# Kernel tuning notes

Measured on AMD Instinct MI355X. Metric: run time of the kernel, lower is better.

Reference implementation:

```python
import jax, jax.numpy as jnp
import numpy as np

N_FEATURES = 1024
N_HEADS = 16
D_ATTN = 64


def setup_inputs() -> dict:
    key = jax.random.key(0)
    k_x, k_qkv, k_pw, k_pb = jax.random.split(key, 4)
    B, S = 2, 2048
    x = jax.random.normal(k_x, (B, S, N_FEATURES), dtype=jnp.float32)
    # torch nn.Linear weights are [out, in]; init scale ~ 1/sqrt(in)
    w_qkv = jax.random.normal(k_qkv, (3 * N_HEADS * D_ATTN, N_FEATURES), dtype=jnp.float32) / np.sqrt(N_FEATURES)
    w_proj = jax.random.normal(k_pw, (N_FEATURES, N_HEADS * D_ATTN), dtype=jnp.float32) / np.sqrt(N_HEADS * D_ATTN)
    b_proj = jax.random.normal(k_pb, (N_FEATURES,), dtype=jnp.float32) / np.sqrt(N_HEADS * D_ATTN)
    return {"x": x, "w_qkv": w_qkv, "w_proj": w_proj, "b_proj": b_proj}


def reference(x, w_qkv, w_proj, b_proj):
    B, S, F = x.shape
    H, D = N_HEADS, D_ATTN
    # fused QKV projection (bias=False): [B,S,3*H*D]
    qkv = jnp.einsum('bsf,of->bso', x, w_qkv)
    qkv = qkv.reshape(B, S, 3, H, D)
    q = jnp.transpose(qkv[:, :, 0], (0, 2, 1, 3))  # [B,H,S,D]
    k = jnp.transpose(qkv[:, :, 1], (0, 2, 1, 3))
    v = jnp.transpose(qkv[:, :, 2], (0, 2, 1, 3))
    scale = 1.0 / jnp.sqrt(jnp.asarray(D, dtype=x.dtype))
    scores = jnp.einsum('bhqd,bhkd->bhqk', q, k) * scale  # [B,H,S,S]
    attn = jax.nn.softmax(scores, axis=-1)
    out = jnp.einsum('bhqk,bhkd->bhqd', attn, v)  # [B,H,S,D]
    out = jnp.transpose(out, (0, 2, 1, 3)).reshape(B, S, H * D)
    # output projection (dropout is identity in eval mode)
    return jnp.einsum('bsm,fm->bsf', out, w_proj) + b_proj
```

## Files before the change

kernel.cpp:

```cpp
#include <hip/hip_runtime.h>
#include <hip/hip_bf16.h>
#include <math.h>

#define BATCH 2
#define SEQ 2048
#define NFEAT 1024
#define NHEAD 16
#define DHEAD 64
#define MROWS (BATCH * SEQ)
#define NQKV (3 * NHEAD * DHEAD)

typedef __attribute__((ext_vector_type(8))) short short8;
typedef __attribute__((ext_vector_type(4))) float floatx4;
typedef __attribute__((ext_vector_type(16))) float floatx16;
typedef __attribute__((ext_vector_type(4))) unsigned int uintx4;

#define CEXP 0.18033688f

__device__ __forceinline__ unsigned short f2bf(float f) {
    unsigned int u = __float_as_uint(f);
    u += 0x7fff + ((u >> 16) & 1);
    return (unsigned short)(u >> 16);
}

__device__ __forceinline__ float fast_exp2(float x) {
    return __builtin_amdgcn_exp2f(x);
}

__device__ __forceinline__ uint pack_bf16x2(float lo, float hi) {
    float2 t; t.x = lo; t.y = hi;
    __hip_bfloat162 h = __float22bfloat162_rn(t);
    union { __hip_bfloat162 h; uint u; } c; c.h = h;
    return c.u;
}

__device__ __forceinline__ void async16(const void* g, void* l) {
    __builtin_amdgcn_global_load_lds(
        (const __attribute__((address_space(1))) void*)g,
        (__attribute__((address_space(3))) void*)l, 16, 0, 0);
}

__global__ void cvt_swz(const float* __restrict__ x, const float* __restrict__ wq,
                        const float* __restrict__ wp,
                        ushort* __restrict__ xb, ushort* __restrict__ wqb,
                        ushort* __restrict__ wpb) {
    const int NX = MROWS * NFEAT / 4, NWQ = NQKV * NFEAT / 4, NWP = NFEAT * NFEAT / 4;
    int i = blockIdx.x * blockDim.x + threadIdx.x;
    if (i >= NX + NWQ + NWP) return;
    const float* src; ushort* dst; int idx4;
    if (i < NX)            { src = x;  dst = xb;  idx4 = i; }
    else if (i < NX + NWQ) { src = wq; dst = wqb; idx4 = i - NX; }
    else                   { src = wp; dst = wpb; idx4 = i - NX - NWQ; }
    float4 v = ((const float4*)src)[idx4];
    ushort4 o;
    o.x = f2bf(v.x); o.y = f2bf(v.y); o.z = f2bf(v.z); o.w = f2bf(v.w);
    const int e = idx4 * 4;
    const int k = e & (NFEAT - 1);
    const int row = e >> 10;
    const int kp = (k & ~31) | (((((k >> 3) & 3) ^ ((row >> 1) & 3))) << 3) | (k & 7);
    *(ushort4*)(dst + (size_t)row * NFEAT + kp) = o;
}

__global__ __launch_bounds__(256, 3)
void gemm_qkv(const ushort* __restrict__ A, const ushort* __restrict__ W,
              ushort* __restrict__ qb, ushort* __restrict__ kb, ushort* __restrict__ vtb) {
    __shared__ ushort smem[16384];
    ushort* As = smem;
    ushort* Bs = smem + 8192;
    const int tid = threadIdx.x;
    const int wave = tid >> 6, lane = tid & 63;
    const int id = blockIdx.x;
    const int xcd = id & 7, slot = id >> 3;
    const int by = (xcd >> 1) * 8 + slot / 12;
    const int bx = (xcd & 1) * 12 + slot % 12;
    const int m0 = by * 128, n0 = bx * 128;
    const int wm = (wave >> 1) * 64, wn = (wave & 1) * 64;
    const int lr = lane & 15, lg = lane >> 4;
    const int kswz = (lg ^ ((lr >> 1) & 3)) * 8;

    floatx4 acc[4][4] = {};

    for (int k0 = 0; k0 < NFEAT; k0 += 64) {
#pragma unroll
        for (int q = 0; q < 4; ++q) {
            const int s = q * 256 + tid;
            const int row = s >> 3, kc = (s & 7) * 8;
            async16(A + (size_t)(m0 + row) * NFEAT + k0 + kc, (void*)(As + s * 8));
            async16(W + (size_t)(n0 + row) * NFEAT + k0 + kc, (void*)(Bs + s * 8));
        }
        __syncthreads();
#pragma unroll
        for (int kk = 0; kk < 2; ++kk) {
            short8 a[4], b[4];
#pragma unroll
            for (int i = 0; i < 4; ++i)
                a[i] = *(const short8*)(As + (wm + i * 16 + lr) * 64 + kk * 32 + kswz);
#pragma unroll
            for (int j = 0; j < 4; ++j)
                b[j] = *(const short8*)(Bs + (wn + j * 16 + lr) * 64 + kk * 32 + kswz);
#pragma unroll
            for (int i = 0; i < 4; ++i)
#pragma unroll
                for (int j = 0; j < 4; ++j)
                    acc[i][j] = __builtin_amdgcn_mfma_f32_16x16x32_bf16(a[i], b[j], acc[i][j], 0, 0, 0);
        }
        __syncthreads();
    }

    const int t = n0 >> 10;
    const int bidx = m0 >> 11;
    if (t < 2) {
#pragma unroll
        for (int i = 0; i < 4; ++i)
#pragma unroll
            for (int j = 0; j < 4; ++j)
#pragma unroll
                for (int r = 0; r < 4; ++r) {
                    const int m = m0 + wm + i * 16 + lg * 4 + r;
                    const int n = n0 + wn + j * 16 + lr;
                    const int s = m & (SEQ - 1);
                    const int rem = n & 1023, h = rem >> 6, d = rem & 63;
                    if (t == 0) {
                        qb[((size_t)(bidx * NHEAD + h) * SEQ + s) * DHEAD + d] =
                            f2bf(acc[i][j][r] * CEXP);
                    } else {
                        const int dcol = ((((d >> 3) ^ (s & 7)) << 3)) | (d & 7);
                        kb[((size_t)(bidx * NHEAD + h) * SEQ + s) * DHEAD + dcol] =
                            f2bf(acc[i][j][r]);
                    }
                }
    } else {
#pragma unroll
        for (int hhalf = 0; hhalf < 2; ++hhalf) {
            if ((wm >> 6) == hhalf) {
#pragma unroll
                for (int i = 0; i < 4; ++i) {
                    const int chunk = i * 2 + (lg >> 1);
#pragma unroll
                    for (int j = 0; j < 4; ++j) {
                        const int n = wn + j * 16 + lr;
                        uint2 pk;
                        pk.x = pack_bf16x2(acc[i][j][0], acc[i][j][1]);
                        pk.y = pack_bf16x2(acc[i][j][2], acc[i][j][3]);
                        *(uint2*)(smem + n * 64 + ((chunk ^ (n & 7)) * 8) + (lg & 1) * 4) = pk;
                    }
                }
            }
            __syncthreads();
            const int s_base = (m0 & (SEQ - 1)) + hhalf * 64;
#pragma unroll
            for (int it = 0; it < 4; ++it) {
                const int n_r = (tid >> 3) + it * 32;
                const int p = tid & 7;
                short8 rowv = *(const short8*)(smem + n_r * 64 + p * 8);
                const int nglob = n0 + n_r;
                const int d = nglob & 63, hh = (nglob & 1023) >> 6;
                *(short8*)(vtb + ((size_t)(bidx * NHEAD + hh) * DHEAD + d) * SEQ + s_base + p * 8) = rowv;
            }
            __syncthreads();
        }
    }
}

__global__ __launch_bounds__(256, 2)
void gemm_proj(const ushort* __restrict__ A, const ushort* __restrict__ W,
               const float* __restrict__ bias, float* __restrict__ Cout) {
    __shared__ ushort As[128 * 64];
    __shared__ ushort Bs[64 * 64];
    const int tid = threadIdx.x;
    const int wave = tid >> 6, lane = tid & 63;
    const int id = blockIdx.x;
    const int xcd = id & 7, slot = id >> 3;
    const int by = (xcd >> 1) * 8 + (slot >> 3);
    const int bx = (xcd & 1) * 8 + (slot & 7);
    const int m0 = by * 128, n0 = bx * 64;
    const int wm = (wave >> 1) * 64, wn = (wave & 1) * 32;
    const int lr = lane & 15, lg = lane >> 4;
    const int kswz = (lg ^ ((lr >> 1) & 3)) * 8;

    floatx4 acc[4][2] = {};

    for (int k0 = 0; k0 < NFEAT; k0 += 64) {
#pragma unroll
        for (int q = 0; q < 4; ++q) {
            const int s = q * 256 + tid;
            const int row = s >> 3, kc = (s & 7) * 8;
            async16(A + (size_t)(m0 + row) * NFEAT + k0 + kc, (void*)(As + s * 8));
        }
#pragma unroll
        for (int q = 0; q < 2; ++q) {
            const int s = q * 256 + tid;
            const int row = s >> 3, kc = (s & 7) * 8;
            async16(W + (size_t)(n0 + row) * NFEAT + k0 + kc, (void*)(Bs + s * 8));
        }
        __syncthreads();
#pragma unroll
        for (int kk = 0; kk < 2; ++kk) {
            short8 a[4], b[2];
#pragma unroll
            for (int i = 0; i < 4; ++i)
                a[i] = *(const short8*)(As + (wm + i * 16 + lr) * 64 + kk * 32 + kswz);
#pragma unroll
            for (int j = 0; j < 2; ++j)
                b[j] = *(const short8*)(Bs + (wn + j * 16 + lr) * 64 + kk * 32 + kswz);
#pragma unroll
            for (int i = 0; i < 4; ++i)
#pragma unroll
                for (int j = 0; j < 2; ++j)
                    acc[i][j] = __builtin_amdgcn_mfma_f32_16x16x32_bf16(a[i], b[j], acc[i][j], 0, 0, 0);
        }
        __syncthreads();
    }

#pragma unroll
    for (int i = 0; i < 4; ++i)
#pragma unroll
        for (int j = 0; j < 2; ++j)
#pragma unroll
            for (int r = 0; r < 4; ++r) {
                const int m = m0 + wm + i * 16 + lg * 4 + r;
                const int n = n0 + wn + j * 16 + lr;
                Cout[(size_t)m * NFEAT + n] = acc[i][j][r] + bias[n];
            }
}

__global__ __launch_bounds__(512, 4)
void flash_attn(const ushort* __restrict__ qb, const ushort* __restrict__ kb,
                const ushort* __restrict__ vtb, ushort* __restrict__ aob) {
    const int id = blockIdx.x;
    const int xcd = id & 7, slot = id >> 3;
    const int bh = xcd + 8 * (slot >> 4);
    const int qt = slot & 15;
    const int tid = threadIdx.x, wave = tid >> 6, lane = tid & 63;
    const int l31 = lane & 31, l5 = lane >> 5;
    const int swz = lane & 7;
    const int kvh = wave >> 2;
    const int qw = wave & 3;

    __shared__ ushort Ks[2][2][64 * 64];
    __shared__ ushort Vs[2][2][64 * 64];

    const ushort* Qb = qb + (size_t)bh * SEQ * DHEAD;
    const ushort* Kb = kb + (size_t)bh * SEQ * DHEAD;
    const ushort* Vt = vtb + (size_t)bh * DHEAD * SEQ;

    const int q0 = qt * 128 + qw * 32;

    short8 qf[4];
#pragma unroll
    for (int kw = 0; kw < 4; ++kw)
        qf[kw] = *(const short8*)(Qb + (size_t)(q0 + l31) * DHEAD + kw * 16 + l5 * 8);

    const int kofs = tid * 8;
    const size_t vrow = (size_t)(tid >> 3) * SEQ;
    const int vcol = (tid & 7) * 8;

    const ushort* KsW = &Ks[kvh][0][0];
    const ushort* VsW = &Vs[kvh][0][0];

    floatx16 acc_o[2] = {};
    float l_lane = 0.0f;

#define FLASH_PREFETCH(BUF, KV)                                                     \
    {                                                                               \
        const int kv_ = (KV);                                                       \
        async16(Kb + (size_t)kv_ * DHEAD + kofs,            (void*)(Ks[0][BUF] + kofs)); \
        async16(Kb + (size_t)(1024 + kv_) * DHEAD + kofs,   (void*)(Ks[1][BUF] + kofs)); \
        async16(Vt + vrow + kv_ + vcol,                     (void*)(Vs[0][BUF] + kofs)); \
        async16(Vt + vrow + 1024 + kv_ + vcol,              (void*)(Vs[1][BUF] + kofs)); \
    }

#define FLASH_COMPUTE(BUF)                                                          \
    {                                                                               \
        floatx16 st[2] = {};                                                        \
        __builtin_amdgcn_s_setprio(1);                                              \
        _Pragma("unroll")                                                           \
        for (int kw = 0; kw < 4; ++kw) {                                            \
            _Pragma("unroll")                                                       \
            for (int i = 0; i < 2; ++i) {                                           \
                short8 kf = *(const short8*)(KsW + (BUF) * 4096 + (i * 32 + l31) * 64 + \
                                             (((kw * 2 + l5) ^ swz) * 8));          \
                st[i] = __builtin_amdgcn_mfma_f32_32x32x16_bf16(kf, qf[kw], st[i], 0, 0, 0); \
            }                                                                       \
        }                                                                           \
        __builtin_amdgcn_s_setprio(0);                                              \
        uintx4 pa[4];                                                               \
        _Pragma("unroll")                                                           \
        for (int i = 0; i < 2; ++i) {                                               \
            uint P2[8];                                                             \
            _Pragma("unroll")                                                       \
            for (int rr = 0; rr < 8; ++rr) {                                        \
                const float p0 = fast_exp2(st[i][rr * 2]);                          \
                const float p1 = fast_exp2(st[i][rr * 2 + 1]);                      \
                l_lane += p0 + p1;                                                  \
                P2[rr] = pack_bf16x2(p0, p1);                                       \
            }                                                                       \
            _Pragma("unroll")                                                       \
            for (int r3 = 0; r3 < 2; ++r3) {                                        \
                _Pragma("unroll")                                                   \
                for (int r1 = 0; r1 < 2; ++r1) {                                    \
                    uint a = P2[r3 * 4 + r1];                            \
                    uint b = P2[r3 * 4 + 2 + r1];                        \
                    asm volatile("v_permlane32_swap_b32 %0, %1" : "+v"(a), "+v"(b)); \
                    pa[i * 2 + r3][r1] = a;               \
                    pa[i * 2 + r3][2 + r1] = b;           \
                }                                                                   \
            }                                                                       \
        }                                                                           \
        __builtin_amdgcn_s_setprio(1);                                              \
        _Pragma("unroll")                                                           \
        for (int kk = 0; kk < 4; ++kk) {                                            \
            const short8 paf = *(const short8*)&pa[kk];                             \
            _Pragma("unroll")                                                       \
            for (int j2 = 0; j2 < 2; ++j2) {                                        \
                short8 vf = *(const short8*)(VsW + (BUF) * 4096 + (j2 * 32 + l31) * 64 + \
                                             (((kk * 2 + l5) ^ swz) * 8));          \
                acc_o[j2] = __builtin_amdgcn_mfma_f32_32x32x16_bf16(paf, vf, acc_o[j2], 0, 0, 0); \
            }                                                                       \
        }                                                                           \
        __builtin_amdgcn_s_setprio(0);                                              \
    }

    FLASH_PREFETCH(0, 0)

    for (int kt = 0; kt < 1024; kt += 128) {
        __syncthreads();
        FLASH_PREFETCH(1, kt + 64)
        FLASH_COMPUTE(0)
        __syncthreads();
        if (kt + 128 < 1024)
            FLASH_PREFETCH(0, kt + 128)
        FLASH_COMPUTE(1)
    }
#undef FLASH_PREFETCH
#undef FLASH_COMPUTE

    __syncthreads();
    float* mrg = (float*)&Ks[0][0][0];
    if (wave >= 4) {
        float* p = mrg + (size_t)(wave - 4) * 2304 + lane * 36;
#pragma unroll
        for (int j2 = 0; j2 < 2; ++j2)
#pragma unroll
            for (int r4 = 0; r4 < 4; ++r4) {
                floatx4 v;
                v[0] = acc_o[j2][r4 * 4 + 0];
                v[1] = acc_o[j2][r4 * 4 + 1];
                v[2] = acc_o[j2][r4 * 4 + 2];
                v[3] = acc_o[j2][r4 * 4 + 3];
                *(floatx4*)(p + j2 * 16 + r4 * 4) = v;
            }
        p[32] = l_lane;
    }
    __syncthreads();
    if (wave < 4) {
        const float* p = mrg + (size_t)wave * 2304 + lane * 36;
#pragma unroll
        for (int j2 = 0; j2 < 2; ++j2)
#pragma unroll
            for (int r4 = 0; r4 < 4; ++r4) {
                floatx4 v = *(const floatx4*)(p + j2 * 16 + r4 * 4);
#pragma unroll
                for (int e = 0; e < 4; ++e)
                    acc_o[j2][r4 * 4 + e] += v[e];
            }
        l_lane += p[32];

        l_lane += __shfl_xor(l_lane, 32);
        const float invl = 1.0f / l_lane;

        const int b = bh >> 4, h = bh & 15;
#pragma unroll
        for (int r = 0; r < 16; ++r) {
            const int qrow = (r & 3) + 4 * l5 + 8 * (r >> 2);
            const float il = __shfl(invl, qrow);
            const int srow = b * SEQ + q0 + qrow;
            const int key = (srow >> 1) & 3;
#pragma unroll
            for (int j2 = 0; j2 < 2; ++j2) {
                const int d = j2 * 32 + l31;
                const int dsw = (d & ~31) | ((((d >> 3) & 3) ^ key) << 3) | (d & 7);
                aob[(size_t)srow * (NHEAD * DHEAD) + h * DHEAD + dsw] = f2bf(acc_o[j2][r] * il);
            }
        }
    }
}

extern "C" void kernel_launch(void* const* d_in, const int* in_sizes, int n_in,
                              void* d_out, int out_size, void* d_ws, size_t ws_size,
                              hipStream_t stream) {
    const float* x      = (const float*)d_in[0];
    const float* w_qkv  = (const float*)d_in[1];
    const float* w_proj = (const float*)d_in[2];
    const float* b_proj = (const float*)d_in[3];
    float* out = (float*)d_out;

    ushort* ws = (ushort*)d_ws;
    ushort* xb     = ws;
    ushort* wqkvb  = xb + (size_t)MROWS * NFEAT;
    ushort* wprojb = wqkvb + (size_t)NQKV * NFEAT;
    ushort* qb     = wprojb + (size_t)NFEAT * NFEAT;
    ushort* kb     = qb + (size_t)MROWS * NFEAT;
    ushort* vtb    = kb + (size_t)MROWS * NFEAT;
    ushort* aob    = vtb + (size_t)MROWS * NFEAT;

    {
        const int total = (MROWS * NFEAT + NQKV * NFEAT + NFEAT * NFEAT) / 4;
        cvt_swz<<<(total + 255) / 256, 256, 0, stream>>>(x, w_qkv, w_proj, xb, wqkvb, wprojb);
    }

    {
        gemm_qkv<<<768, 256, 0, stream>>>(xb, wqkvb, qb, kb, vtb);
    }

    {
        flash_attn<<<512, 512, 0, stream>>>(qb, kb, vtb, aob);
    }

    {
        gemm_proj<<<512, 256, 0, stream>>>(aob, wprojb, b_proj, out);
    }
}
```

Before: 176.2 us.

## Halve flash-attention waves, each wave handles 64 query rows sharing K/V fragments

The attention block drops from 8 to 4 waves. Each wave now processes two 32-row query sub-tiles, so every K and V fragment read from LDS feeds two MFMAs instead of one. This halves LDS read traffic per unit of compute and doubles register use per wave for accumulators and Q fragments. Each thread now issues twice as many async prefetch loads, and the merge step is reworked for the new wave layout. The risk is lower occupancy and less latency hiding with fewer waves per block.

```diff
diff --git a/kernel.cpp b/kernel.cpp
--- a/kernel.cpp
+++ b/kernel.cpp
@@ -224,7 +224,7 @@
             }
 }
 
-__global__ __launch_bounds__(512, 4)
+__global__ __launch_bounds__(256, 2)
 void flash_attn(const ushort* __restrict__ qb, const ushort* __restrict__ kb,
                 const ushort* __restrict__ vtb, ushort* __restrict__ aob) {
     const int id = blockIdx.x;
@@ -234,45 +234,52 @@
     const int tid = threadIdx.x, wave = tid >> 6, lane = tid & 63;
     const int l31 = lane & 31, l5 = lane >> 5;
     const int swz = lane & 7;
-    const int kvh = wave >> 2;
-    const int qw = wave & 3;
-
-    __shared__ ushort Ks[2][2][64 * 64];
-    __shared__ ushort Vs[2][2][64 * 64];
+    const int kvh = wave >> 1;
+    const int qw = wave & 1;
+
+    __shared__ __align__(16) ushort sm[32768];
+    ushort* Ksp = sm;
+    ushort* Vsp = sm + 16384;
 
     const ushort* Qb = qb + (size_t)bh * SEQ * DHEAD;
     const ushort* Kb = kb + (size_t)bh * SEQ * DHEAD;
     const ushort* Vt = vtb + (size_t)bh * DHEAD * SEQ;
 
-    const int q0 = qt * 128 + qw * 32;
-
-    short8 qf[4];
-#pragma unroll
-    for (int kw = 0; kw < 4; ++kw)
-        qf[kw] = *(const short8*)(Qb + (size_t)(q0 + l31) * DHEAD + kw * 16 + l5 * 8);
+    const int q0 = qt * 128 + qw * 64;
+
+    short8 qf[2][4];
+#pragma unroll
+    for (int qh = 0; qh < 2; ++qh)
+#pragma unroll
+        for (int kw = 0; kw < 4; ++kw)
+            qf[qh][kw] = *(const short8*)(Qb + (size_t)(q0 + qh * 32 + l31) * DHEAD + kw * 16 + l5 * 8);
 
     const int kofs = tid * 8;
     const size_t vrow = (size_t)(tid >> 3) * SEQ;
     const int vcol = (tid & 7) * 8;
 
-    const ushort* KsW = &Ks[kvh][0][0];
-    const ushort* VsW = &Vs[kvh][0][0];
-
-    floatx16 acc_o[2] = {};
-    float l_lane = 0.0f;
+    const ushort* KsW = Ksp + kvh * 8192;
+    const ushort* VsW = Vsp + kvh * 8192;
+
+    floatx16 acc_o[2][2] = {};
+    float l_lane[2] = {0.0f, 0.0f};
 
 #define FLASH_PREFETCH(BUF, KV)                                                     \
     {                                                                               \
         const int kv_ = (KV);                                                       \
-        async16(Kb + (size_t)kv_ * DHEAD + kofs,            (void*)(Ks[0][BUF] + kofs)); \
-        async16(Kb + (size_t)(1024 + kv_) * DHEAD + kofs,   (void*)(Ks[1][BUF] + kofs)); \
-        async16(Vt + vrow + kv_ + vcol,                     (void*)(Vs[0][BUF] + kofs)); \
-        async16(Vt + vrow + 1024 + kv_ + vcol,              (void*)(Vs[1][BUF] + kofs)); \
+        async16(Kb + (size_t)kv_ * DHEAD + kofs,                 (void*)(Ksp + (BUF) * 4096 + kofs)); \
+        async16(Kb + (size_t)kv_ * DHEAD + 2048 + kofs,          (void*)(Ksp + (BUF) * 4096 + 2048 + kofs)); \
+        async16(Kb + (size_t)(1024 + kv_) * DHEAD + kofs,        (void*)(Ksp + 8192 + (BUF) * 4096 + kofs)); \
+        async16(Kb + (size_t)(1024 + kv_) * DHEAD + 2048 + kofs, (void*)(Ksp + 8192 + (BUF) * 4096 + 2048 + kofs)); \
+        async16(Vt + vrow + kv_ + vcol,                          (void*)(Vsp + (BUF) * 4096 + kofs)); \
+        async16(Vt + 32 * SEQ + vrow + kv_ + vcol,               (void*)(Vsp + (BUF) * 4096 + 2048 + kofs)); \
+        async16(Vt + vrow + 1024 + kv_ + vcol,                   (void*)(Vsp + 8192 + (BUF) * 4096 + kofs)); \
+        async16(Vt + 32 * SEQ + vrow + 1024 + kv_ + vcol,        (void*)(Vsp + 8192 + (BUF) * 4096 + 2048 + kofs)); \
     }
 
 #define FLASH_COMPUTE(BUF)                                                          \
     {                                                                               \
-        floatx16 st[2] = {};                                                        \
+        floatx16 st[2][2] = {};                                                     \
         __builtin_amdgcn_s_setprio(1);                                              \
         _Pragma("unroll")                                                           \
         for (int kw = 0; kw < 4; ++kw) {                                            \
@@ -280,42 +287,48 @@
             for (int i = 0; i < 2; ++i) {                                           \
                 short8 kf = *(const short8*)(KsW + (BUF) * 4096 + (i * 32 + l31) * 64 + \
                                              (((kw * 2 + l5) ^ swz) * 8));          \
-                st[i] = __builtin_amdgcn_mfma_f32_32x32x16_bf16(kf, qf[kw], st[i], 0, 0, 0); \
+                st[0][i] = __builtin_amdgcn_mfma_f32_32x32x16_bf16(kf, qf[0][kw], st[0][i], 0, 0, 0); \
+                st[1][i] = __builtin_amdgcn_mfma_f32_32x32x16_bf16(kf, qf[1][kw], st[1][i], 0, 0, 0); \
             }                                                                       \
         }                                                                           \
         __builtin_amdgcn_s_setprio(0);                                              \
-        uintx4 pa[4];                                                               \
+        uintx4 pa[2][4];                                                            \
         _Pragma("unroll")                                                           \
-        for (int i = 0; i < 2; ++i) {                                               \
-            uint P2[8];                                                             \
+        for (int qh = 0; qh < 2; ++qh) {                                            \
             _Pragma("unroll")                                                       \
-            for (int rr = 0; rr < 8; ++rr) {                                        \
-                const float p0 = fast_exp2(st[i][rr * 2]);                          \
-                const float p1 = fast_exp2(st[i][rr * 2 + 1]);                      \
-                l_lane += p0 + p1;                                                  \
-                P2[rr] = pack_bf16x2(p0, p1);                                       \
-            }                                                                       \
-            _Pragma("unroll")                                                       \
-            for (int r3 = 0; r3 < 2; ++r3) {                                        \
+            for (int i = 0; i < 2; ++i) {                                           \
+                uint P2[8];                                                         \
                 _Pragma("unroll")                                                   \
-                for (int r1 = 0; r1 < 2; ++r1) {                                    \
-                    uint a = P2[r3 * 4 + r1];                            \
-                    uint b = P2[r3 * 4 + 2 + r1];                        \
-                    asm volatile("v_permlane32_swap_b32 %0, %1" : "+v"(a), "+v"(b)); \
-                    pa[i * 2 + r3][r1] = a;               \
-                    pa[i * 2 + r3][2 + r1] = b;           \
+                for (int rr = 0; rr < 8; ++rr) {                                    \
+                    const float p0 = fast_exp2(st[qh][i][rr * 2]);                  \
+                    const float p1 = fast_exp2(st[qh][i][rr * 2 + 1]);              \
+                    l_lane[qh] += p0 + p1;                                          \
+                    P2[rr] = pack_bf16x2(p0, p1);                                   \
+                }                                                                   \
+                _Pragma("unroll")                                                   \
+                for (int r3 = 0; r3 < 2; ++r3) {                                    \
+                    _Pragma("unroll")                                               \
+                    for (int r1 = 0; r1 < 2; ++r1) {                                \
+                        uint a = P2[r3 * 4 + r1];                        \
+                        uint b = P2[r3 * 4 + 2 + r1];                    \
+                        asm volatile("v_permlane32_swap_b32 %0, %1" : "+v"(a), "+v"(b)); \
+                        pa[qh][i * 2 + r3][r1] = a;       \
+                        pa[qh][i * 2 + r3][2 + r1] = b;   \
+                    }                                                               \
                 }                                                                   \
             }                                                                       \
         }                                                                           \
         __builtin_amdgcn_s_setprio(1);                                              \
         _Pragma("unroll")                                                           \
         for (int kk = 0; kk < 4; ++kk) {                                            \
-            const short8 paf = *(const short8*)&pa[kk];                             \
+            const short8 paf0 = *(const short8*)&pa[0][kk];                         \
+            const short8 paf1 = *(const short8*)&pa[1][kk];                         \
             _Pragma("unroll")                                                       \
             for (int j2 = 0; j2 < 2; ++j2) {                                        \
                 short8 vf = *(const short8*)(VsW + (BUF) * 4096 + (j2 * 32 + l31) * 64 + \
                                              (((kk * 2 + l5) ^ swz) * 8));          \
-                acc_o[j2] = __builtin_amdgcn_mfma_f32_32x32x16_bf16(paf, vf, acc_o[j2], 0, 0, 0); \
+                acc_o[0][j2] = __builtin_amdgcn_mfma_f32_32x32x16_bf16(paf0, vf, acc_o[0][j2], 0, 0, 0); \
+                acc_o[1][j2] = __builtin_amdgcn_mfma_f32_32x32x16_bf16(paf1, vf, acc_o[1][j2], 0, 0, 0); \
             }                                                                       \
         }                                                                           \
         __builtin_amdgcn_s_setprio(0);                                              \
@@ -336,51 +349,59 @@
 #undef FLASH_COMPUTE
 
     __syncthreads();
-    float* mrg = (float*)&Ks[0][0][0];
-    if (wave >= 4) {
-        float* p = mrg + (size_t)(wave - 4) * 2304 + lane * 36;
-#pragma unroll
-        for (int j2 = 0; j2 < 2; ++j2)
-#pragma unroll
-            for (int r4 = 0; r4 < 4; ++r4) {
-                floatx4 v;
-                v[0] = acc_o[j2][r4 * 4 + 0];
-                v[1] = acc_o[j2][r4 * 4 + 1];
-                v[2] = acc_o[j2][r4 * 4 + 2];
-                v[3] = acc_o[j2][r4 * 4 + 3];
-                *(floatx4*)(p + j2 * 16 + r4 * 4) = v;
-            }
-        p[32] = l_lane;
+    float* Mrg = (float*)sm;
+    if (kvh == 1) {
+        float* p = Mrg + (size_t)(qw * 64 + lane) * 68;
+#pragma unroll
+        for (int qh = 0; qh < 2; ++qh)
+#pragma unroll
+            for (int j2 = 0; j2 < 2; ++j2)
+#pragma unroll
+                for (int r4 = 0; r4 < 4; ++r4) {
+                    floatx4 v;
+                    v[0] = acc_o[qh][j2][r4 * 4 + 0];
+                    v[1] = acc_o[qh][j2][r4 * 4 + 1];
+                    v[2] = acc_o[qh][j2][r4 * 4 + 2];
+                    v[3] = acc_o[qh][j2][r4 * 4 + 3];
+                    *(floatx4*)(p + qh * 32 + j2 * 16 + r4 * 4) = v;
+                }
+        p[64] = l_lane[0];
+        p[65] = l_lane[1];
     }
     __syncthreads();
-    if (wave < 4) {
-        const float* p = mrg + (size_t)wave * 2304 + lane * 36;
-#pragma unroll
-        for (int j2 = 0; j2 < 2; ++j2)
-#pragma unroll
-            for (int r4 = 0; r4 < 4; ++r4) {
-                floatx4 v = *(const floatx4*)(p + j2 * 16 + r4 * 4);
-#pragma unroll
-                for (int e = 0; e < 4; ++e)
-                    acc_o[j2][r4 * 4 + e] += v[e];
-            }
-        l_lane += p[32];
-
-        l_lane += __shfl_xor(l_lane, 32);
-        const float invl = 1.0f / l_lane;
+    if (kvh == 0) {
+        const float* p = Mrg + (size_t)(qw * 64 + lane) * 68;
+#pragma unroll
+        for (int qh = 0; qh < 2; ++qh)
+#pragma unroll
+            for (int j2 = 0; j2 < 2; ++j2)
+#pragma unroll
+                for (int r4 = 0; r4 < 4; ++r4) {
+                    floatx4 v = *(const floatx4*)(p + qh * 32 + j2 * 16 + r4 * 4);
+#pragma unroll
+                    for (int e = 0; e < 4; ++e)
+                        acc_o[qh][j2][r4 * 4 + e] += v[e];
+                }
+        l_lane[0] += p[64];
+        l_lane[1] += p[65];
 
         const int b = bh >> 4, h = bh & 15;
 #pragma unroll
-        for (int r = 0; r < 16; ++r) {
-            const int qrow = (r & 3) + 4 * l5 + 8 * (r >> 2);
-            const float il = __shfl(invl, qrow);
-            const int srow = b * SEQ + q0 + qrow;
-            const int key = (srow >> 1) & 3;
-#pragma unroll
-            for (int j2 = 0; j2 < 2; ++j2) {
-                const int d = j2 * 32 + l31;
-                const int dsw = (d & ~31) | ((((d >> 3) & 3) ^ key) << 3) | (d & 7);
-                aob[(size_t)srow * (NHEAD * DHEAD) + h * DHEAD + dsw] = f2bf(acc_o[j2][r] * il);
+        for (int qh = 0; qh < 2; ++qh) {
+            l_lane[qh] += __shfl_xor(l_lane[qh], 32);
+            const float invl = 1.0f / l_lane[qh];
+#pragma unroll
+            for (int r = 0; r < 16; ++r) {
+                const int qrow = (r & 3) + 4 * l5 + 8 * (r >> 2);
+                const float il = __shfl(invl, qrow);
+                const int srow = b * SEQ + q0 + qh * 32 + qrow;
+                const int key = (srow >> 1) & 3;
+#pragma unroll
+                for (int j2 = 0; j2 < 2; ++j2) {
+                    const int d = j2 * 32 + l31;
+                    const int dsw = (d & ~31) | ((((d >> 3) & 3) ^ key) << 3) | (d & 7);
+                    aob[(size_t)srow * (NHEAD * DHEAD) + h * DHEAD + dsw] = f2bf(acc_o[qh][j2][r] * il);
+                }
             }
         }
     }
@@ -414,7 +435,7 @@
     }
 
     {
-        flash_attn<<<512, 512, 0, stream>>>(qb, kb, vtb, aob);
+        flash_attn<<<512, 256, 0, stream>>>(qb, kb, vtb, aob);
     }
 
     {
```

Measured after the change: 180.6 us. +2.5%, slower.

## Drop LDS staging in flash attention and read K/V directly from global

Applied to the files above, without the earlier changes.

The attention kernel no longer stages K and V tiles in shared memory through double-buffered async copies. Each wave now loads its K and V MFMA fragments straight from global memory, relying on the existing swizzled layout and on L2/cache hits. Blocks shrink to four waves covering 64 queries, with twice as many blocks launched, and shared memory is kept only for the final merge of the two KV halves. This cuts LDS use and the copy pipeline, which allows more resident blocks. The cost is exposed global-load latency, no reuse of K/V tiles across waves in a block, and a barrier left inside the loop.

```diff
diff --git a/kernel.cpp b/kernel.cpp
--- a/kernel.cpp
+++ b/kernel.cpp
@@ -224,121 +224,88 @@
             }
 }
 
-__global__ __launch_bounds__(512, 4)
+__global__ __launch_bounds__(256, 4)
 void flash_attn(const ushort* __restrict__ qb, const ushort* __restrict__ kb,
                 const ushort* __restrict__ vtb, ushort* __restrict__ aob) {
     const int id = blockIdx.x;
     const int xcd = id & 7, slot = id >> 3;
-    const int bh = xcd + 8 * (slot >> 4);
-    const int qt = slot & 15;
+    const int bh = xcd + 8 * (slot >> 5);
+    const int qt2 = slot & 31;
     const int tid = threadIdx.x, wave = tid >> 6, lane = tid & 63;
     const int l31 = lane & 31, l5 = lane >> 5;
-    const int swz = lane & 7;
-    const int kvh = wave >> 2;
-    const int qw = wave & 3;
-
-    __shared__ ushort Ks[2][2][64 * 64];
-    __shared__ ushort Vs[2][2][64 * 64];
+    const int swz = l31 & 7;
+    const int kvh = wave >> 1;
+    const int qw = wave & 1;
+
+    __shared__ float mrg[2 * 64 * 36];
 
     const ushort* Qb = qb + (size_t)bh * SEQ * DHEAD;
-    const ushort* Kb = kb + (size_t)bh * SEQ * DHEAD;
-    const ushort* Vt = vtb + (size_t)bh * DHEAD * SEQ;
-
-    const int q0 = qt * 128 + qw * 32;
+    const ushort* Kb = kb + (size_t)bh * SEQ * DHEAD + (size_t)kvh * 1024 * DHEAD;
+    const ushort* Vt = vtb + (size_t)bh * DHEAD * SEQ + (size_t)kvh * 1024;
+
+    const int q0 = qt2 * 64 + qw * 32;
 
     short8 qf[4];
 #pragma unroll
     for (int kw = 0; kw < 4; ++kw)
         qf[kw] = *(const short8*)(Qb + (size_t)(q0 + l31) * DHEAD + kw * 16 + l5 * 8);
 
-    const int kofs = tid * 8;
-    const size_t vrow = (size_t)(tid >> 3) * SEQ;
-    const int vcol = (tid & 7) * 8;
-
-    const ushort* KsW = &Ks[kvh][0][0];
-    const ushort* VsW = &Vs[kvh][0][0];
-
     floatx16 acc_o[2] = {};
     float l_lane = 0.0f;
 
-#define FLASH_PREFETCH(BUF, KV)                                                     \
-    {                                                                               \
-        const int kv_ = (KV);                                                       \
-        async16(Kb + (size_t)kv_ * DHEAD + kofs,            (void*)(Ks[0][BUF] + kofs)); \
-        async16(Kb + (size_t)(1024 + kv_) * DHEAD + kofs,   (void*)(Ks[1][BUF] + kofs)); \
-        async16(Vt + vrow + kv_ + vcol,                     (void*)(Vs[0][BUF] + kofs)); \
-        async16(Vt + vrow + 1024 + kv_ + vcol,              (void*)(Vs[1][BUF] + kofs)); \
-    }
-
-#define FLASH_COMPUTE(BUF)                                                          \
-    {                                                                               \
-        floatx16 st[2] = {};                                                        \
-        __builtin_amdgcn_s_setprio(1);                                              \
-        _Pragma("unroll")                                                           \
-        for (int kw = 0; kw < 4; ++kw) {                                            \
-            _Pragma("unroll")                                                       \
-            for (int i = 0; i < 2; ++i) {                                           \
-                short8 kf = *(const short8*)(KsW + (BUF) * 4096 + (i * 32 + l31) * 64 + \
-                                             (((kw * 2 + l5) ^ swz) * 8));          \
-                st[i] = __builtin_amdgcn_mfma_f32_32x32x16_bf16(kf, qf[kw], st[i], 0, 0, 0); \
-            }                                                                       \
-        }                                                                           \
-        __builtin_amdgcn_s_setprio(0);                                              \
-        uintx4 pa[4];                                                               \
-        _Pragma("unroll")                                                           \
-        for (int i = 0; i < 2; ++i) {                                               \
-            uint P2[8];                                                             \
-            _Pragma("unroll")                                                       \
-            for (int rr = 0; rr < 8; ++rr) {                                        \
-                const float p0 = fast_exp2(st[i][rr * 2]);                          \
-                const float p1 = fast_exp2(st[i][rr * 2 + 1]);                      \
-                l_lane += p0 + p1;                                                  \
-                P2[rr] = pack_bf16x2(p0, p1);                                       \
-            }                                                                       \
-            _Pragma("unroll")                                                       \
-            for (int r3 = 0; r3 < 2; ++r3) {                                        \
-                _Pragma("unroll")                                                   \
-                for (int r1 = 0; r1 < 2; ++r1) {                                    \
-                    uint a = P2[r3 * 4 + r1];                            \
-                    uint b = P2[r3 * 4 + 2 + r1];                        \
-                    asm volatile("v_permlane32_swap_b32 %0, %1" : "+v"(a), "+v"(b)); \
-                    pa[i * 2 + r3][r1] = a;               \
-                    pa[i * 2 + r3][2 + r1] = b;           \
-                }                                                                   \
-            }                                                                       \
-        }                                                                           \
-        __builtin_amdgcn_s_setprio(1);                                              \
-        _Pragma("unroll")                                                           \
-        for (int kk = 0; kk < 4; ++kk) {                                            \
-            const short8 paf = *(const short8*)&pa[kk];                             \
-            _Pragma("unroll")                                                       \
-            for (int j2 = 0; j2 < 2; ++j2) {                                        \
-                short8 vf = *(const short8*)(VsW + (BUF) * 4096 + (j2 * 32 + l31) * 64 + \
-                                             (((kk * 2 + l5) ^ swz) * 8));          \
-                acc_o[j2] = __builtin_amdgcn_mfma_f32_32x32x16_bf16(paf, vf, acc_o[j2], 0, 0, 0); \
-            }                                                                       \
-        }                                                                           \
-        __builtin_amdgcn_s_setprio(0);                                              \
-    }
-
-    FLASH_PREFETCH(0, 0)
-
-    for (int kt = 0; kt < 1024; kt += 128) {
-        __syncthreads();
-        FLASH_PREFETCH(1, kt + 64)
-        FLASH_COMPUTE(0)
-        __syncthreads();
-        if (kt + 128 < 1024)
-            FLASH_PREFETCH(0, kt + 128)
-        FLASH_COMPUTE(1)
-    }
-#undef FLASH_PREFETCH
-#undef FLASH_COMPUTE
-
-    __syncthreads();
-    float* mrg = (float*)&Ks[0][0][0];
-    if (wave >= 4) {
-        float* p = mrg + (size_t)(wave - 4) * 2304 + lane * 36;
+    for (int kt = 0; kt < 1024; kt += 64) {
+        floatx16 st[2] = {};
+        __builtin_amdgcn_s_setprio(1);
+#pragma unroll
+        for (int kw = 0; kw < 4; ++kw) {
+#pragma unroll
+            for (int i = 0; i < 2; ++i) {
+                short8 kf = *(const short8*)(Kb + (size_t)(kt + i * 32 + l31) * DHEAD +
+                                             (((kw * 2 + l5) ^ swz) * 8));
+                st[i] = __builtin_amdgcn_mfma_f32_32x32x16_bf16(kf, qf[kw], st[i], 0, 0, 0);
+            }
+        }
+        __builtin_amdgcn_s_setprio(0);
+        uintx4 pa[4];
+#pragma unroll
+        for (int i = 0; i < 2; ++i) {
+            uint P2[8];
+#pragma unroll
+            for (int rr = 0; rr < 8; ++rr) {
+                const float p0 = fast_exp2(st[i][rr * 2]);
+                const float p1 = fast_exp2(st[i][rr * 2 + 1]);
+                l_lane += p0 + p1;
+                P2[rr] = pack_bf16x2(p0, p1);
+            }
+#pragma unroll
+            for (int r3 = 0; r3 < 2; ++r3) {
+#pragma unroll
+                for (int r1 = 0; r1 < 2; ++r1) {
+                    uint a = P2[r3 * 4 + r1];
+                    uint b = P2[r3 * 4 + 2 + r1];
+                    asm volatile("v_permlane32_swap_b32 %0, %1" : "+v"(a), "+v"(b));
+                    pa[i * 2 + r3][r1] = a;
+                    pa[i * 2 + r3][2 + r1] = b;
+                }
+            }
+        }
+        __builtin_amdgcn_s_setprio(1);
+#pragma unroll
+        for (int kk = 0; kk < 4; ++kk) {
+            const short8 paf = *(const short8*)&pa[kk];
+#pragma unroll
+            for (int j2 = 0; j2 < 2; ++j2) {
+                short8 vf = *(const short8*)(Vt + (size_t)(j2 * 32 + l31) * SEQ + kt +
+                                             (((kk * 2 + l5) ^ swz) * 8));
+                acc_o[j2] = __builtin_amdgcn_mfma_f32_32x32x16_bf16(paf, vf, acc_o[j2], 0, 0, 0);
+            }
+        }
+        __builtin_amdgcn_s_setprio(0);
+        __syncthreads();
+    }
+
+    float* p = mrg + (size_t)(qw * 64 + lane) * 36;
+    if (kvh == 1) {
 #pragma unroll
         for (int j2 = 0; j2 < 2; ++j2)
 #pragma unroll
@@ -353,8 +320,7 @@
         p[32] = l_lane;
     }
     __syncthreads();
-    if (wave < 4) {
-        const float* p = mrg + (size_t)wave * 2304 + lane * 36;
+    if (kvh == 0) {
 #pragma unroll
         for (int j2 = 0; j2 < 2; ++j2)
 #pragma unroll
@@ -414,7 +380,7 @@
     }
 
     {
-        flash_attn<<<512, 512, 0, stream>>>(qb, kb, vtb, aob);
+        flash_attn<<<1024, 256, 0, stream>>>(qb, kb, vtb, aob);
     }
 
     {
```

New measurement: 199.8 us. +13.4%, slower.

## Load V fragments directly from global memory instead of staging through LDS

Applied to the files above, without the earlier changes.

The flash-attention kernel stops copying V tiles into shared memory. Each wave now reads its V MFMA operands straight from global (transposed V) memory, with half of them issued early in the compute step to hide latency. Shared memory shrinks to the K buffers plus the merge scratch, which may allow more resident blocks. In exchange there is more global/L2 traffic, because each of the four q-waves reloads the same V data, and the loads sit on the critical path before the PV MFMAs.

```diff
diff --git a/kernel.cpp b/kernel.cpp
--- a/kernel.cpp
+++ b/kernel.cpp
@@ -233,16 +233,16 @@
     const int qt = slot & 15;
     const int tid = threadIdx.x, wave = tid >> 6, lane = tid & 63;
     const int l31 = lane & 31, l5 = lane >> 5;
-    const int swz = lane & 7;
+    const int swz = l31 & 7;
     const int kvh = wave >> 2;
     const int qw = wave & 3;
 
-    __shared__ ushort Ks[2][2][64 * 64];
-    __shared__ ushort Vs[2][2][64 * 64];
+    __shared__ __align__(16) char smraw[36864];
+    ushort* Ksp = (ushort*)smraw;
 
     const ushort* Qb = qb + (size_t)bh * SEQ * DHEAD;
     const ushort* Kb = kb + (size_t)bh * SEQ * DHEAD;
-    const ushort* Vt = vtb + (size_t)bh * DHEAD * SEQ;
+    const ushort* Vt = vtb + (size_t)bh * DHEAD * SEQ + (size_t)kvh * 1024;
 
     const int q0 = qt * 128 + qw * 32;
 
@@ -252,11 +252,7 @@
         qf[kw] = *(const short8*)(Qb + (size_t)(q0 + l31) * DHEAD + kw * 16 + l5 * 8);
 
     const int kofs = tid * 8;
-    const size_t vrow = (size_t)(tid >> 3) * SEQ;
-    const int vcol = (tid & 7) * 8;
-
-    const ushort* KsW = &Ks[kvh][0][0];
-    const ushort* VsW = &Vs[kvh][0][0];
+    const ushort* KsW = Ksp + kvh * 8192;
 
     floatx16 acc_o[2] = {};
     float l_lane = 0.0f;
@@ -264,14 +260,20 @@
 #define FLASH_PREFETCH(BUF, KV)                                                     \
     {                                                                               \
         const int kv_ = (KV);                                                       \
-        async16(Kb + (size_t)kv_ * DHEAD + kofs,            (void*)(Ks[0][BUF] + kofs)); \
-        async16(Kb + (size_t)(1024 + kv_) * DHEAD + kofs,   (void*)(Ks[1][BUF] + kofs)); \
-        async16(Vt + vrow + kv_ + vcol,                     (void*)(Vs[0][BUF] + kofs)); \
-        async16(Vt + vrow + 1024 + kv_ + vcol,              (void*)(Vs[1][BUF] + kofs)); \
-    }
-
-#define FLASH_COMPUTE(BUF)                                                          \
+        async16(Kb + (size_t)kv_ * DHEAD + kofs,          (void*)(Ksp + (BUF) * 4096 + kofs));        \
+        async16(Kb + (size_t)(1024 + kv_) * DHEAD + kofs, (void*)(Ksp + 8192 + (BUF) * 4096 + kofs)); \
+    }
+
+#define FLASH_COMPUTE(BUF, KV)                                                      \
     {                                                                               \
+                    \
+        short8 vgA[2][2];                                                           \
+        _Pragma("unroll")                                                           \
+        for (int kk = 0; kk < 2; ++kk)                                              \
+            _Pragma("unroll")                                                       \
+            for (int j2 = 0; j2 < 2; ++j2)                                          \
+                vgA[kk][j2] = *(const short8*)(Vt + (size_t)(j2 * 32 + l31) * SEQ + \
+                                               (KV) + (((kk * 2 + l5) ^ swz) * 8)); \
         floatx16 st[2] = {};                                                        \
         __builtin_amdgcn_s_setprio(1);                                              \
         _Pragma("unroll")                                                           \
@@ -313,8 +315,9 @@
             const short8 paf = *(const short8*)&pa[kk];                             \
             _Pragma("unroll")                                                       \
             for (int j2 = 0; j2 < 2; ++j2) {                                        \
-                short8 vf = *(const short8*)(VsW + (BUF) * 4096 + (j2 * 32 + l31) * 64 + \
-                                             (((kk * 2 + l5) ^ swz) * 8));          \
+                short8 vf = (kk < 2) ? vgA[kk][j2]                                  \
+                    : *(const short8*)(Vt + (size_t)(j2 * 32 + l31) * SEQ + (KV) +  \
+                                       (((kk * 2 + l5) ^ swz) * 8));                \
                 acc_o[j2] = __builtin_amdgcn_mfma_f32_32x32x16_bf16(paf, vf, acc_o[j2], 0, 0, 0); \
             }                                                                       \
         }                                                                           \
@@ -326,19 +329,19 @@
     for (int kt = 0; kt < 1024; kt += 128) {
         __syncthreads();
         FLASH_PREFETCH(1, kt + 64)
-        FLASH_COMPUTE(0)
+        FLASH_COMPUTE(0, kt)
         __syncthreads();
         if (kt + 128 < 1024)
             FLASH_PREFETCH(0, kt + 128)
-        FLASH_COMPUTE(1)
+        FLASH_COMPUTE(1, kt + 64)
     }
 #undef FLASH_PREFETCH
 #undef FLASH_COMPUTE
 
     __syncthreads();
-    float* mrg = (float*)&Ks[0][0][0];
-    if (wave >= 4) {
-        float* p = mrg + (size_t)(wave - 4) * 2304 + lane * 36;
+    float* mrg = (float*)smraw;
+    float* p = mrg + (size_t)(qw * 64 + lane) * 36;
+    if (kvh == 1) {
 #pragma unroll
         for (int j2 = 0; j2 < 2; ++j2)
 #pragma unroll
@@ -353,8 +356,7 @@
         p[32] = l_lane;
     }
     __syncthreads();
-    if (wave < 4) {
-        const float* p = mrg + (size_t)wave * 2304 + lane * 36;
+    if (kvh == 0) {
 #pragma unroll
         for (int j2 = 0; j2 < 2; ++j2)
 #pragma unroll
```

New measurement: 212.1 us. 1.2x slower.
